# Kernel optimization log

Measured on AMD Instinct MI355X. Metric: run time of the kernel, lower is better.

## Reference

```python
import jax, jax.numpy as jnp
import numpy as np

EPS = 1e-5

def setup_inputs() -> dict:
    key = jax.random.key(0)
    ks = jax.random.split(key, 10)
    B, C, H, W, D = 1, 128, 20, 20, 20
    Cq = C // 8
    s = 0.05
    return {
        "x":   jax.random.normal(ks[0], (B, C, H, W, D), jnp.float32),
        "wq":  jax.random.normal(ks[1], (Cq, C), jnp.float32) * s,
        "bq":  jnp.zeros((Cq,), jnp.float32),
        "wk":  jax.random.normal(ks[2], (Cq, C), jnp.float32) * s,
        "bk":  jnp.zeros((Cq,), jnp.float32),
        "wv":  jax.random.normal(ks[3], (C, C), jnp.float32) * s,
        "bv":  jnp.zeros((C,), jnp.float32),
        "wa":  jax.random.normal(ks[4], (C, C), jnp.float32) * s,
        "ba":  jnp.zeros((C,), jnp.float32),
        "bn_w": jnp.ones((C,), jnp.float32),
        "bn_b": jnp.zeros((C,), jnp.float32),
    }

def reference(x, wq, bq, wk, bk, wv, bv, wa, ba, bn_w, bn_b):
    B, C, H, W, D = x.shape
    N = H * W * D
    xf = x.reshape(B, C, N)                                   # (B,C,N)
    # 1x1 conv projections = per-position channel matmuls
    q = jnp.einsum('oc,bcn->bno', wq, xf) + bq                # (B,N,Cq)
    k = jnp.einsum('oc,bcn->bon', wk, xf) + bk[:, None]       # (B,Cq,N)
    v = jnp.einsum('oc,bcn->bon', wv, xf) + bv[:, None]       # (B,C,N)
    # raw (unscaled) attention, softmax over key positions
    att = jax.nn.softmax(jnp.einsum('bnc,bcm->bnm', q, k), axis=-1)  # (B,N,N)
    # att_value[b,c,i] = sum_j value[b,c,j] * att[b,i,j]
    av = jnp.einsum('bcj,bij->bci', v, att)                   # (B,C,N)
    y = jnp.einsum('oc,bcn->bon', wa, av) + ba[:, None]       # (B,C,N)
    # BatchNorm (training mode): per-channel stats over batch + spatial
    mean = jnp.mean(y, axis=(0, 2), keepdims=True)
    var = jnp.var(y, axis=(0, 2), keepdims=True)
    y = (y - mean) * jax.lax.rsqrt(var + EPS) * bn_w[:, None] + bn_b[:, None]
    out = jax.nn.relu(y) + xf
    return out.reshape(B, C, H, W, D)
```

## Files before the change

kernel.cpp:

```cpp
#include <hip/hip_runtime.h>
#include <math.h>

#define N_POS 8000
#define C_CH  128
#define KSPLIT 5
#define KT_PER 25
#define QTILES 125

typedef __bf16 bf16x8 __attribute__((ext_vector_type(8)));
typedef float  f32x4  __attribute__((ext_vector_type(4)));

#define MFMA(a,b,c) __builtin_amdgcn_mfma_f32_16x16x32_bf16((a),(b),(c),0,0,0)


#define GLOAD_LDS(gp, lp) \
    __builtin_amdgcn_global_load_lds( \
        (const __attribute__((address_space(1))) void*)(gp), \
        (__attribute__((address_space(3))) void*)(lp), 16, 0, 0)

__global__ __launch_bounds__(256) void qkv_kernel(
    const float* __restrict__ x,
    const float* __restrict__ wq, const float* __restrict__ bq,
    const float* __restrict__ wk, const float* __restrict__ bk,
    const float* __restrict__ wv, const float* __restrict__ bv,
    __bf16* __restrict__ q_bf, __bf16* __restrict__ k_bf, __bf16* __restrict__ v_bf)
{
    __shared__ __bf16 x_lds[32 * 136];
    __shared__ __bf16 v_out[128 * 36];

    const int t    = threadIdx.x;
    const int n0   = blockIdx.x * 32;
    const int lane = t & 63;
    const int w    = t >> 6;
    const int l15  = lane & 15;
    const int quad = lane >> 4;

    for (int r = 0; r < 4; ++r) {
        int f = r * 256 + t;
        int ch = f >> 3, n4 = f & 7;
        float4 xv = *reinterpret_cast<const float4*>(&x[ch * N_POS + n0 + n4 * 4]);
        x_lds[(n4 * 4 + 0) * 136 + ch] = (__bf16)xv.x;
        x_lds[(n4 * 4 + 1) * 136 + ch] = (__bf16)xv.y;
        x_lds[(n4 * 4 + 2) * 136 + ch] = (__bf16)xv.z;
        x_lds[(n4 * 4 + 3) * 136 + ch] = (__bf16)xv.w;
    }

    bf16x8 aw[3][4];
    f32x4  acc[3][2];
    const int nmt = (w < 2) ? 3 : 2;
    for (int mi = 0; mi < nmt; ++mi) {
        int mt = w + 4 * mi;
        const float *wrow, *brow;
        if (mt == 0)      { wrow = wq + l15 * 128;               brow = bq; }
        else if (mt == 1) { wrow = wk + l15 * 128;               brow = bk; }
        else              { wrow = wv + ((mt - 2) * 16 + l15) * 128;
                            brow = bv + (mt - 2) * 16; }
        for (int ks = 0; ks < 4; ++ks) {
            float4 f0 = *reinterpret_cast<const float4*>(wrow + ks * 32 + quad * 8);
            float4 f1 = *reinterpret_cast<const float4*>(wrow + ks * 32 + quad * 8 + 4);
            bf16x8 a;
            a[0]=(__bf16)f0.x; a[1]=(__bf16)f0.y; a[2]=(__bf16)f0.z; a[3]=(__bf16)f0.w;
            a[4]=(__bf16)f1.x; a[5]=(__bf16)f1.y; a[6]=(__bf16)f1.z; a[7]=(__bf16)f1.w;
            aw[mi][ks] = a;
        }
        for (int ni = 0; ni < 2; ++ni) {
            acc[mi][ni][0] = brow[quad * 4 + 0]; acc[mi][ni][1] = brow[quad * 4 + 1];
            acc[mi][ni][2] = brow[quad * 4 + 2]; acc[mi][ni][3] = brow[quad * 4 + 3];
        }
    }
    __syncthreads();

    for (int ks = 0; ks < 4; ++ks) {
        bf16x8 b0 = *reinterpret_cast<const bf16x8*>(&x_lds[(0  + l15) * 136 + ks * 32 + quad * 8]);
        bf16x8 b1 = *reinterpret_cast<const bf16x8*>(&x_lds[(16 + l15) * 136 + ks * 32 + quad * 8]);
        for (int mi = 0; mi < nmt; ++mi) {
            acc[mi][0] = MFMA(aw[mi][ks], b0, acc[mi][0]);
            acc[mi][1] = MFMA(aw[mi][ks], b1, acc[mi][1]);
        }
    }

    union S4 { short4 s; __bf16 b[4]; };
    for (int mi = 0; mi < nmt; ++mi) {
        int mt = w + 4 * mi;
        for (int ni = 0; ni < 2; ++ni) {
            S4 u;
            u.b[0]=(__bf16)acc[mi][ni][0]; u.b[1]=(__bf16)acc[mi][ni][1];
            u.b[2]=(__bf16)acc[mi][ni][2]; u.b[3]=(__bf16)acc[mi][ni][3];
            int n = n0 + ni * 16 + l15;
            if (mt == 0) {
                *reinterpret_cast<short4*>(&q_bf[n * 16 + quad * 4]) = u.s;
            } else if (mt == 1) {
                *reinterpret_cast<short4*>(&k_bf[n * 16 + quad * 4]) = u.s;
            } else {
                int ch0 = (mt - 2) * 16 + quad * 4;
                int nl  = ni * 16 + l15;
                v_out[(ch0 + 0) * 36 + nl] = u.b[0];
                v_out[(ch0 + 1) * 36 + nl] = u.b[1];
                v_out[(ch0 + 2) * 36 + nl] = u.b[2];
                v_out[(ch0 + 3) * 36 + nl] = u.b[3];
            }
        }
    }
    __syncthreads();
    for (int r = 0; r < 4; ++r) {
        int f = r * 256 + t;
        int ch = f >> 3, n4 = f & 7;
        int2 d = *reinterpret_cast<const int2*>(&v_out[ch * 36 + n4 * 4]);
        *reinterpret_cast<int2*>(&v_bf[ch * N_POS + n0 + n4 * 4]) = d;
    }
}

__global__ __launch_bounds__(256, 3) void attn_kernel(
    const __bf16* __restrict__ q_bf, const __bf16* __restrict__ k_bf,
    const __bf16* __restrict__ v_bf, float* __restrict__ av_part,
    float* __restrict__ l_part)
{
    __shared__ __bf16 v_buf[2][8192];
    __shared__ __bf16 p_lds[2][4096];

    const int t    = threadIdx.x;
    const int qt   = blockIdx.x % QTILES;
    const int sp   = blockIdx.x / QTILES;
    const int n0q  = qt * 64;
    const int lane = t & 63;
    const int w    = t >> 6;
    const int l15  = lane & 15;
    const int quad = lane >> 4;

    const int chL   = lane >> 3;
    const int vpart = (lane & 7) ^ chL;

    bf16x8 aq[4];
    for (int ni = 0; ni < 4; ++ni) {
        for (int j = 0; j < 8; ++j) aq[ni][j] = (__bf16)0.0f;
        if (quad < 2)
            aq[ni] = *reinterpret_cast<const bf16x8*>(
                &q_bf[(n0q + ni * 16 + l15) * 16 + quad * 8]);
    }

    f32x4 acc[2][4];
    for (int mi = 0; mi < 2; ++mi)
        for (int ni = 0; ni < 4; ++ni)
            for (int r = 0; r < 4; ++r) acc[mi][ni][r] = 0.f;
    float lp[4] = {0.f, 0.f, 0.f, 0.f};

    const int kt0   = sp * KT_PER;
    const int ktEnd = kt0 + KT_PER;

    auto stageV = [&](int kt) {
        const int n0k = kt * 64;
        __bf16* vb = &v_buf[kt & 1][0];
        for (int r = 0; r < 4; ++r) {
            int R = w * 4 + r;
            GLOAD_LDS(v_bf + (8 * R + chL) * N_POS + n0k + vpart * 8,
                      &vb[R * 512]);
        }
    };

    bf16x8 kA, kB;
    for (int j = 0; j < 8; ++j) { kA[j] = (__bf16)0.0f; kB[j] = (__bf16)0.0f; }

    stageV(kt0);
    if (quad < 2)
        kA = *reinterpret_cast<const bf16x8*>(
            &k_bf[(size_t)(kt0 * 64 + w * 16 + l15) * 16 + quad * 8]);

    const int oS  = w * 2 + (quad >> 1);
    const int sub = (quad & 1) * 4;

    union S4 { short4 sh; __bf16 b[4]; };

    auto iter = [&](int kt, bf16x8& kc, bf16x8& kn, int pbuf) {
        const bool last = (kt + 1 >= ktEnd);
        if (!last) {
            stageV(kt + 1);
            if (quad < 2)
                kn = *reinterpret_cast<const bf16x8*>(
                    &k_bf[(size_t)((kt + 1) * 64 + w * 16 + l15) * 16 + quad * 8]);
            asm volatile("s_waitcnt vmcnt(5)" ::: "memory");
        } else {
            asm volatile("s_waitcnt vmcnt(0)" ::: "memory");
        }
        __builtin_amdgcn_sched_barrier(0);

        __bf16* pb = &p_lds[pbuf][0];
#pragma unroll
        for (int ni = 0; ni < 4; ++ni) {
            f32x4 s;
            for (int r = 0; r < 4; ++r) s[r] = 0.f;
            s = MFMA(kc, aq[ni], s);
            S4 u;
            u.b[0] = (__bf16)__expf(s[0]); u.b[1] = (__bf16)__expf(s[1]);
            u.b[2] = (__bf16)__expf(s[2]); u.b[3] = (__bf16)__expf(s[3]);
            *reinterpret_cast<short4*>(
                &pb[(oS * 64 + ni * 16 + l15) * 8 + sub]) = u.sh;
            lp[ni] += (float)u.b[0] + (float)u.b[1]
                    + (float)u.b[2] + (float)u.b[3];
        }

        asm volatile("s_waitcnt lgkmcnt(0)" ::: "memory");
        __builtin_amdgcn_s_barrier();
        __builtin_amdgcn_sched_barrier(0);

        const __bf16* vb = &v_buf[kt & 1][0];
        const __bf16* pr = &p_lds[pbuf][0];
        const int chl = l15 & 7;
#pragma unroll
        for (int ks = 0; ks < 2; ++ks) {
            int pz = ((ks * 4 + quad) ^ chl);
            bf16x8 a0 = *reinterpret_cast<const bf16x8*>(
                &vb[(((2 * w)     * 2 + (l15 >> 3)) * 64 + chl * 8 + pz) * 8]);
            bf16x8 a1 = *reinterpret_cast<const bf16x8*>(
                &vb[(((2 * w + 1) * 2 + (l15 >> 3)) * 64 + chl * 8 + pz) * 8]);
            const int ob = (ks * 4 + quad) * 64;
            bf16x8 p0 = *reinterpret_cast<const bf16x8*>(&pr[(ob +  0 + l15) * 8]);
            bf16x8 p1 = *reinterpret_cast<const bf16x8*>(&pr[(ob + 16 + l15) * 8]);
            bf16x8 p2 = *reinterpret_cast<const bf16x8*>(&pr[(ob + 32 + l15) * 8]);
            bf16x8 p3 = *reinterpret_cast<const bf16x8*>(&pr[(ob + 48 + l15) * 8]);
            acc[0][0] = MFMA(a0, p0, acc[0][0]);
            acc[0][1] = MFMA(a0, p1, acc[0][1]);
            acc[0][2] = MFMA(a0, p2, acc[0][2]);
            acc[0][3] = MFMA(a0, p3, acc[0][3]);
            acc[1][0] = MFMA(a1, p0, acc[1][0]);
            acc[1][1] = MFMA(a1, p1, acc[1][1]);
            acc[1][2] = MFMA(a1, p2, acc[1][2]);
            acc[1][3] = MFMA(a1, p3, acc[1][3]);
        }
    };

    for (int i = 0; i < KT_PER; i += 2) {
        iter(kt0 + i, kA, kB, 0);
        if (i + 1 < KT_PER) iter(kt0 + i + 1, kB, kA, 1);
    }

    __syncthreads();
    float* lsh = reinterpret_cast<float*>(&p_lds[0][0]);
    float lt[4];
#pragma unroll
    for (int ni = 0; ni < 4; ++ni) {
        float ps = lp[ni];
        ps += __shfl_xor(ps, 16, 64);
        ps += __shfl_xor(ps, 32, 64);
        lt[ni] = ps;
    }
    if (quad == 0) {
#pragma unroll
        for (int ni = 0; ni < 4; ++ni)
            lsh[w * 64 + ni * 16 + l15] = lt[ni];
    }
    __syncthreads();

    float* dst = av_part + (size_t)sp * 1024000;
    for (int mi = 0; mi < 2; ++mi)
        for (int ni = 0; ni < 4; ++ni) {
            int n  = n0q + ni * 16 + l15;
            int ch = (2 * w + mi) * 16 + quad * 4;
            *reinterpret_cast<f32x4*>(&dst[n * 128 + ch]) = acc[mi][ni];
        }
    if (t < 64)
        l_part[sp * N_POS + n0q + t] =
            lsh[t] + lsh[64 + t] + lsh[128 + t] + lsh[192 + t];
}

__global__ __launch_bounds__(256) void proj_out_kernel(
    const float* __restrict__ av_part, const float* __restrict__ l_part,
    const float* __restrict__ wa, const float* __restrict__ ba,
    float* __restrict__ y_ws, float* __restrict__ bn_sum, float* __restrict__ bn_sumsq)
{
    __shared__ __bf16 b_lds[4096];

    const int t    = threadIdx.x;
    const int n0   = blockIdx.x * 32;
    const int lane = t & 63;
    const int w    = t >> 6;
    const int l15  = lane & 15;
    const int quad = lane >> 4;

    for (int r = 0; r < 2; ++r) {
        int g = r * 256 + t;
        int n = g >> 4, oc = g & 15;
        float l = 0.f;
#pragma unroll
        for (int s = 0; s < KSPLIT; ++s) l += l_part[s * N_POS + n0 + n];
        float4 a0 = make_float4(0.f, 0.f, 0.f, 0.f);
        float4 a1 = make_float4(0.f, 0.f, 0.f, 0.f);
#pragma unroll
        for (int s = 0; s < KSPLIT; ++s) {
            const float* p = av_part + (size_t)s * 1024000 + (n0 + n) * 128 + oc * 8;
            float4 u = *reinterpret_cast<const float4*>(p);
            float4 v = *reinterpret_cast<const float4*>(p + 4);
            a0.x += u.x; a0.y += u.y; a0.z += u.z; a0.w += u.w;
            a1.x += v.x; a1.y += v.y; a1.z += v.z; a1.w += v.w;
        }
        float inv = 1.f / l;
        union { int4 iv; __bf16 b[8]; } u;
        u.b[0]=(__bf16)(a0.x*inv); u.b[1]=(__bf16)(a0.y*inv);
        u.b[2]=(__bf16)(a0.z*inv); u.b[3]=(__bf16)(a0.w*inv);
        u.b[4]=(__bf16)(a1.x*inv); u.b[5]=(__bf16)(a1.y*inv);
        u.b[6]=(__bf16)(a1.z*inv); u.b[7]=(__bf16)(a1.w*inv);
        int A = (n >> 4) * 16 + oc;
        int slot = (n & 15) ^ (oc & 7);
        *reinterpret_cast<int4*>(&b_lds[(A * 16 + slot) * 8]) = u.iv;
    }

    bf16x8 aw[2][4];
    f32x4  acc[2][2];
    for (int mi = 0; mi < 2; ++mi) {
        int mt = 2 * w + mi;
        const float* wrow = wa + (mt * 16 + l15) * 128;
        for (int ks = 0; ks < 4; ++ks) {
            float4 f0 = *reinterpret_cast<const float4*>(wrow + ks * 32 + quad * 8);
            float4 f1 = *reinterpret_cast<const float4*>(wrow + ks * 32 + quad * 8 + 4);
            bf16x8 a;
            a[0]=(__bf16)f0.x; a[1]=(__bf16)f0.y; a[2]=(__bf16)f0.z; a[3]=(__bf16)f0.w;
            a[4]=(__bf16)f1.x; a[5]=(__bf16)f1.y; a[6]=(__bf16)f1.z; a[7]=(__bf16)f1.w;
            aw[mi][ks] = a;
        }
        for (int ni = 0; ni < 2; ++ni) {
            acc[mi][ni][0] = ba[mt * 16 + quad * 4 + 0];
            acc[mi][ni][1] = ba[mt * 16 + quad * 4 + 1];
            acc[mi][ni][2] = ba[mt * 16 + quad * 4 + 2];
            acc[mi][ni][3] = ba[mt * 16 + quad * 4 + 3];
        }
    }
    __syncthreads();

    for (int ks = 0; ks < 4; ++ks) {
        int oc = ks * 4 + quad;
        int slot = l15 ^ (oc & 7);
        bf16x8 b0 = *reinterpret_cast<const bf16x8*>(&b_lds[((0  + oc) * 16 + slot) * 8]);
        bf16x8 b1 = *reinterpret_cast<const bf16x8*>(&b_lds[((16 + oc) * 16 + slot) * 8]);
        for (int mi = 0; mi < 2; ++mi) {
            acc[mi][0] = MFMA(aw[mi][ks], b0, acc[mi][0]);
            acc[mi][1] = MFMA(aw[mi][ks], b1, acc[mi][1]);
        }
    }

    for (int mi = 0; mi < 2; ++mi) {
        for (int r = 0; r < 4; ++r) {
            int ch = (2 * w + mi) * 16 + quad * 4 + r;
            float v0 = acc[mi][0][r];
            float v1 = acc[mi][1][r];
            y_ws[ch * N_POS + n0 + 0  + l15] = v0;
            y_ws[ch * N_POS + n0 + 16 + l15] = v1;
            float s1 = v0 + v1;
            float s2 = v0 * v0 + v1 * v1;
#pragma unroll
            for (int off = 8; off >= 1; off >>= 1) {
                s1 += __shfl_xor(s1, off, 64);
                s2 += __shfl_xor(s2, off, 64);
            }
            if (l15 == 0) {
                atomicAdd(&bn_sum[ch],   s1);
                atomicAdd(&bn_sumsq[ch], s2);
            }
        }
    }
}

__global__ __launch_bounds__(256) void bn_relu_kernel(
    const float* __restrict__ y_ws, const float* __restrict__ x,
    const float* __restrict__ bn_sum, const float* __restrict__ bn_sumsq,
    const float* __restrict__ bn_w, const float* __restrict__ bn_b,
    float* __restrict__ out)
{
    const int i4 = blockIdx.x * 256 + threadIdx.x;
    const int c  = i4 / 2000;
    const float mean  = bn_sum[c]   * (1.f / 8000.f);
    const float var   = bn_sumsq[c] * (1.f / 8000.f) - mean * mean;
    const float rstd  = rsqrtf(var + 1e-5f);
    const float scale = bn_w[c] * rstd;
    const float shift = bn_b[c] - mean * scale;

    float4 y4 = reinterpret_cast<const float4*>(y_ws)[i4];
    float4 x4 = reinterpret_cast<const float4*>(x)[i4];
    float4 o4;
    o4.x = fmaxf(y4.x * scale + shift, 0.f) + x4.x;
    o4.y = fmaxf(y4.y * scale + shift, 0.f) + x4.y;
    o4.z = fmaxf(y4.z * scale + shift, 0.f) + x4.z;
    o4.w = fmaxf(y4.w * scale + shift, 0.f) + x4.w;
    reinterpret_cast<float4*>(out)[i4] = o4;
}

extern "C" void kernel_launch(void* const* d_in, const int* in_sizes, int n_in,
                              void* d_out, int out_size, void* d_ws, size_t ws_size,
                              hipStream_t stream)
{
    const float* x    = (const float*)d_in[0];
    const float* wq   = (const float*)d_in[1];
    const float* bq   = (const float*)d_in[2];
    const float* wk   = (const float*)d_in[3];
    const float* bk   = (const float*)d_in[4];
    const float* wv   = (const float*)d_in[5];
    const float* bv   = (const float*)d_in[6];
    const float* wa   = (const float*)d_in[7];
    const float* ba   = (const float*)d_in[8];
    const float* bn_w = (const float*)d_in[9];
    const float* bn_b = (const float*)d_in[10];
    float* out = (float*)d_out;

    char* base = (char*)d_ws;
    float*  av_part = (float*)base;
    __bf16* q_bf    = (__bf16*)(base + 20480000);
    __bf16* k_bf    = (__bf16*)(base + 20736000);
    __bf16* v_bf    = (__bf16*)(base + 20992000);
    float*  l_part  = (float*)(base + 23040000);
    float*  bn_sum   = (float*)(base + 23200000);
    float*  bn_sumsq = bn_sum + 128;
    float*  y_ws    = (float*)(base + 23201024);

    hipMemsetAsync(bn_sum, 0, 1024, stream);
    qkv_kernel<<<250, 256, 0, stream>>>(x, wq, bq, wk, bk, wv, bv, q_bf, k_bf, v_bf);
    attn_kernel<<<QTILES * KSPLIT, 256, 0, stream>>>(q_bf, k_bf, v_bf, av_part, l_part);
    proj_out_kernel<<<250, 256, 0, stream>>>(av_part, l_part, wa, ba, y_ws, bn_sum, bn_sumsq);
    bn_relu_kernel<<<1000, 256, 0, stream>>>(y_ws, x, bn_sum, bn_sumsq, bn_w, bn_b, out);
}
```

Measured before the change: 163.3 us.

## Reduce split-K attention partials in last-arriving block via atomic counter

```diff
diff --git a/kernel.cpp b/kernel.cpp
--- a/kernel.cpp
+++ b/kernel.cpp
@@ -113,7 +113,8 @@
 __global__ __launch_bounds__(256, 3) void attn_kernel(
     const __bf16* __restrict__ q_bf, const __bf16* __restrict__ k_bf,
     const __bf16* __restrict__ v_bf, float* __restrict__ av_part,
-    float* __restrict__ l_part)
+    float* __restrict__ l_part, int* __restrict__ cnt,
+    __bf16* __restrict__ av_bf)
 {
     __shared__ __bf16 v_buf[2][8192];
     __shared__ __bf16 p_lds[2][4096];
@@ -260,10 +261,47 @@
     if (t < 64)
         l_part[sp * N_POS + n0q + t] =
             lsh[t] + lsh[64 + t] + lsh[128 + t] + lsh[192 + t];
+
+    __threadfence();
+    __shared__ int last_flag;
+    if (t == 0) {
+        int prev = atomicAdd(&cnt[qt], 1);
+        last_flag = (prev == KSPLIT - 1) ? 1 : 0;
+    }
+    __syncthreads();
+    if (!last_flag) return;
+    __threadfence();
+
+#pragma unroll
+    for (int r = 0; r < 4; ++r) {
+        int g   = r * 256 + t;
+        int row = g >> 4, oc = g & 15;
+        int n   = n0q + row;
+        float l = 0.f;
+#pragma unroll
+        for (int s = 0; s < KSPLIT; ++s) l += l_part[s * N_POS + n];
+        float4 a0 = make_float4(0.f, 0.f, 0.f, 0.f);
+        float4 a1 = make_float4(0.f, 0.f, 0.f, 0.f);
+#pragma unroll
+        for (int s = 0; s < KSPLIT; ++s) {
+            const float* p = av_part + (size_t)s * 1024000 + n * 128 + oc * 8;
+            float4 u = *reinterpret_cast<const float4*>(p);
+            float4 v = *reinterpret_cast<const float4*>(p + 4);
+            a0.x += u.x; a0.y += u.y; a0.z += u.z; a0.w += u.w;
+            a1.x += v.x; a1.y += v.y; a1.z += v.z; a1.w += v.w;
+        }
+        float inv = 1.f / l;
+        union { int4 iv; __bf16 b[8]; } u;
+        u.b[0]=(__bf16)(a0.x*inv); u.b[1]=(__bf16)(a0.y*inv);
+        u.b[2]=(__bf16)(a0.z*inv); u.b[3]=(__bf16)(a0.w*inv);
+        u.b[4]=(__bf16)(a1.x*inv); u.b[5]=(__bf16)(a1.y*inv);
+        u.b[6]=(__bf16)(a1.z*inv); u.b[7]=(__bf16)(a1.w*inv);
+        *reinterpret_cast<int4*>(&av_bf[n * 128 + oc * 8]) = u.iv;
+    }
 }
 
 __global__ __launch_bounds__(256) void proj_out_kernel(
-    const float* __restrict__ av_part, const float* __restrict__ l_part,
+    const __bf16* __restrict__ av_bf,
     const float* __restrict__ wa, const float* __restrict__ ba,
     float* __restrict__ y_ws, float* __restrict__ bn_sum, float* __restrict__ bn_sumsq)
 {
@@ -279,28 +317,10 @@
     for (int r = 0; r < 2; ++r) {
         int g = r * 256 + t;
         int n = g >> 4, oc = g & 15;
-        float l = 0.f;
-#pragma unroll
-        for (int s = 0; s < KSPLIT; ++s) l += l_part[s * N_POS + n0 + n];
-        float4 a0 = make_float4(0.f, 0.f, 0.f, 0.f);
-        float4 a1 = make_float4(0.f, 0.f, 0.f, 0.f);
-#pragma unroll
-        for (int s = 0; s < KSPLIT; ++s) {
-            const float* p = av_part + (size_t)s * 1024000 + (n0 + n) * 128 + oc * 8;
-            float4 u = *reinterpret_cast<const float4*>(p);
-            float4 v = *reinterpret_cast<const float4*>(p + 4);
-            a0.x += u.x; a0.y += u.y; a0.z += u.z; a0.w += u.w;
-            a1.x += v.x; a1.y += v.y; a1.z += v.z; a1.w += v.w;
-        }
-        float inv = 1.f / l;
-        union { int4 iv; __bf16 b[8]; } u;
-        u.b[0]=(__bf16)(a0.x*inv); u.b[1]=(__bf16)(a0.y*inv);
-        u.b[2]=(__bf16)(a0.z*inv); u.b[3]=(__bf16)(a0.w*inv);
-        u.b[4]=(__bf16)(a1.x*inv); u.b[5]=(__bf16)(a1.y*inv);
-        u.b[6]=(__bf16)(a1.z*inv); u.b[7]=(__bf16)(a1.w*inv);
+        int4 u = *reinterpret_cast<const int4*>(&av_bf[(n0 + n) * 128 + oc * 8]);
         int A = (n >> 4) * 16 + oc;
         int slot = (n & 15) ^ (oc & 7);
-        *reinterpret_cast<int4*>(&b_lds[(A * 16 + slot) * 8]) = u.iv;
+        *reinterpret_cast<int4*>(&b_lds[(A * 16 + slot) * 8]) = u;
     }
 
     bf16x8 aw[2][4];
@@ -408,10 +428,13 @@
     float*  bn_sum   = (float*)(base + 23200000);
     float*  bn_sumsq = bn_sum + 128;
     float*  y_ws    = (float*)(base + 23201024);
+    __bf16* av_bf   = (__bf16*)(base + 27297024);
+    int*    cnt     = (int*)(base + 29345024);
 
     hipMemsetAsync(bn_sum, 0, 1024, stream);
+    hipMemsetAsync(cnt, 0, 512, stream);
     qkv_kernel<<<250, 256, 0, stream>>>(x, wq, bq, wk, bk, wv, bv, q_bf, k_bf, v_bf);
-    attn_kernel<<<QTILES * KSPLIT, 256, 0, stream>>>(q_bf, k_bf, v_bf, av_part, l_part);
-    proj_out_kernel<<<250, 256, 0, stream>>>(av_part, l_part, wa, ba, y_ws, bn_sum, bn_sumsq);
+    attn_kernel<<<QTILES * KSPLIT, 256, 0, stream>>>(q_bf, k_bf, v_bf, av_part, l_part, cnt, av_bf);
+    proj_out_kernel<<<250, 256, 0, stream>>>(av_bf, wa, ba, y_ws, bn_sum, bn_sumsq);
     bn_relu_kernel<<<1000, 256, 0, stream>>>(y_ws, x, bn_sum, bn_sumsq, bn_w, bn_b, out);
 }
```

New measurement: 242.6 us. +48.6%, slower.
